# Optimization experiments

Hardware: AMD Instinct MI355X
Metric: run time of the kernel (lower is better)

## Reference

```python
import jax, jax.numpy as jnp
import numpy as np

L_LAYERS, D, H, FF_MUL = 4, 512, 8, 4
VOCAB, SEQ, MEM, CMEM, RATIO = 32000, 1024, 1024, 256, 4
DH = D // H


def _ln(x, g, b):
    mu = jnp.mean(x, -1, keepdims=True)
    var = jnp.mean((x - mu) ** 2, -1, keepdims=True)
    return (x - mu) / jnp.sqrt(var + 1e-5) * g + b


def _heads(x):
    b, n, _ = x.shape
    return x.reshape(b, n, H, -1).transpose(0, 2, 1, 3)  # [b,h,n,dh]


def _shift(x):
    # relative-position shift trick, x: [b,h,i,j] -> [b,h,i,j]
    b, h, i, j = x.shape
    x = jnp.concatenate([x, jnp.zeros((b, h, i, i), x.dtype)], -1)
    l = i + j - 1
    x = x.reshape(b, h, i * (i + j))
    pad = (-x.shape[-1]) % l
    x = jnp.pad(x, ((0, 0), (0, 0), (0, pad))).reshape(b, h, -1, l)
    return x[:, :, :i, i - 1:]


def _conv(x, w, b):
    # x: [B,L,D], w: [D_out, D_in, RATIO] (OIH), stride=RATIO
    y = jax.lax.conv_general_dilated(x.transpose(0, 2, 1), w, (RATIO,), 'VALID',
                                     dimension_numbers=('NCH', 'OIH', 'NCH'))
    return y.transpose(0, 2, 1) + b


def _full_attn(q, k, v):
    dots = jnp.einsum('bhid,bhjd->bhij', q, k) * (q.shape[-1] ** -0.5)
    return jnp.einsum('bhij,bhjd->bhid', jax.nn.softmax(dots, -1), v)


def setup_inputs() -> dict:
    key = jax.random.key(0)
    ks = jax.random.split(key, 24)
    s = 0.02
    return {
        'seq': jax.random.randint(ks[0], (4, SEQ), 0, VOCAB),
        'mask': jnp.ones((4, SEQ), dtype=bool),
        'mems': jax.random.normal(ks[1], (L_LAYERS, 4, MEM, D)) * s,
        'cmems': jax.random.normal(ks[2], (L_LAYERS, 4, CMEM, D)) * s,
        'pos_emb': jax.random.normal(ks[3], (H, CMEM + MEM + SEQ, DH)) * s,
        'embed': jax.random.normal(ks[4], (VOCAB, D)) * s,
        'ln1_g': jnp.ones((L_LAYERS, D)), 'ln1_b': jnp.zeros((L_LAYERS, D)),
        'Wq': jax.random.normal(ks[5], (L_LAYERS, D, D)) * s,
        'Wkv': jax.random.normal(ks[6], (L_LAYERS, D, 2 * D)) * s,
        'Wo': jax.random.normal(ks[7], (L_LAYERS, D, D)) * s,
        'bo': jnp.zeros((L_LAYERS, D)),
        'conv_w': jax.random.normal(ks[8], (L_LAYERS, D, D, RATIO)) * s,
        'conv_b': jnp.zeros((L_LAYERS, D)),
        'ln2_g': jnp.ones((L_LAYERS, D)), 'ln2_b': jnp.zeros((L_LAYERS, D)),
        'W1': jax.random.normal(ks[9], (L_LAYERS, D, FF_MUL * D)) * s,
        'b1': jnp.zeros((L_LAYERS, FF_MUL * D)),
        'W2': jax.random.normal(ks[10], (L_LAYERS, FF_MUL * D, D)) * s,
        'b2': jnp.zeros((L_LAYERS, D)),
    }


def _forward(seq, mask, mems, cmems, pos_emb, embed, ln1_g, ln1_b, Wq, Wkv, Wo, bo,
             conv_w, conv_b, ln2_g, ln2_b, W1, b1, W2, b2):
    scale = DH ** -0.5
    x = embed[seq]  # [b,t,d]
    maskb = mask.astype(bool)
    new_mems, new_cmems = [], []
    aux_total = jnp.zeros((), x.dtype)
    w_acc = 0.0
    for l in range(L_LAYERS):
        mem, cmem = mems[l], cmems[l]
        xn = _ln(x, ln1_g[l], ln1_b[l])
        q = _heads(xn @ Wq[l])
        kv_in = jnp.concatenate([cmem, mem, xn], 1)  # [b,kv_len,d]
        kv_len = kv_in.shape[1]
        k, v = jnp.split(kv_in @ Wkv[l], 2, -1)
        k, v = _heads(k), _heads(v)
        dots = jnp.einsum('bhid,bhjd->bhij', q, k) * scale
        pe = pos_emb[:, -kv_len:]
        dots = dots + _shift(jnp.einsum('bhid,hjd->bhij', q, pe) * scale)
        m2 = maskb[:, None, :, None] & maskb[:, None, None, :]  # [b,1,t,t]
        m2 = jnp.pad(m2, ((0, 0), (0, 0), (0, 0), (kv_len - SEQ, 0)), constant_values=True)
        dots = jnp.where(m2, dots, -jnp.finfo(dots.dtype).max)
        attn = jax.nn.softmax(dots, -1)
        w_acc = w_acc + jnp.mean(jax.lax.stop_gradient(attn), axis=(0, 1))
        out = jnp.einsum('bhij,bhjd->bhid', attn, v)
        out = out.transpose(0, 2, 1, 3).reshape(x.shape[0], SEQ, D)
        x = x + out @ Wo[l] + bo[l]
        # FIFO memory update (queue normed x, evict oldest)
        queue = jnp.concatenate([mem, xn], 1)
        old_mem, new_mem = queue[:, :-MEM], queue[:, -MEM:]
        pad_amt = old_mem.shape[1] % RATIO
        if pad_amt:
            old_mem = jnp.pad(old_mem, ((0, 0), (pad_amt, 0), (0, 0)))
        comp = _conv(old_mem, conv_w[l], conv_b[l])
        new_cmem = jnp.concatenate([cmem, comp], 1)[:, -CMEM:]
        new_mems.append(new_mem)
        new_cmems.append(new_cmem)
        # reconstruction (attention-reconstruction) aux loss
        old_mem_d = jax.lax.stop_gradient(old_mem)
        comp2 = _conv(old_mem_d, conv_w[l], conv_b[l])
        ck, cv = jnp.split(comp2 @ jax.lax.stop_gradient(Wkv[l]), 2, -1)
        ck, cv = _heads(ck), _heads(cv)
        start = kv_len - min(mem.shape[1], MEM) - SEQ
        ok = jax.lax.stop_gradient(k[:, :, start:kv_len - SEQ])
        ov = jax.lax.stop_gradient(v[:, :, start:kv_len - SEQ])
        qd = jax.lax.stop_gradient(q)
        aux_total = aux_total + jnp.mean((_full_attn(qd, ok, ov) - _full_attn(qd, ck, cv)) ** 2)
        # feed-forward block (PreNorm + Residual), exact GELU like torch nn.GELU
        xn2 = _ln(x, ln2_g[l], ln2_b[l])
        x = x + jax.nn.gelu(xn2 @ W1[l] + b1[l], approximate=False) @ W2[l] + b2[l]
    return (x, jnp.stack(new_mems), jnp.stack(new_cmems),
            aux_total / L_LAYERS, w_acc / L_LAYERS)


def reference(seq, mask, mems, cmems, pos_emb, embed, ln1_g, ln1_b, Wq, Wkv, Wo, bo,
              conv_w, conv_b, ln2_g, ln2_b, W1, b1, W2, b2):
    return _forward(seq, mask, mems, cmems, pos_emb, embed, ln1_g, ln1_b, Wq, Wkv, Wo, bo,
                    conv_w, conv_b, ln2_g, ln2_b, W1, b1, W2, b2)
```

## Files before the change

kernel.cpp:

```cpp
#include <hip/hip_runtime.h>
#include <hip/hip_bf16.h>


typedef __hip_bfloat16 bf16;
typedef short s16x8 __attribute__((ext_vector_type(8)));
typedef float f32x4 __attribute__((ext_vector_type(4)));

__device__ __forceinline__ f32x4 mfma16(s16x8 a, s16x8 b, f32x4 c) {
  return __builtin_amdgcn_mfma_f32_16x16x32_bf16(a, b, c, 0, 0, 0);
}

typedef __attribute__((address_space(1))) const void gvoid;
typedef __attribute__((address_space(3))) void lvoid;
__device__ __forceinline__ void gll16(const void* g, void* l) {
  __builtin_amdgcn_global_load_lds((gvoid*)g, (lvoid*)l, 16, 0, 0);
}

__device__ __forceinline__ float b2f(unsigned short u) {
  return __uint_as_float(((unsigned)u) << 16);
}
__device__ __forceinline__ unsigned short f2bb(float f) {
  bf16 h = __float2bfloat16(f);
  return *reinterpret_cast<unsigned short*>(&h);
}
__device__ __forceinline__ float ldf(const float* p) { return *p; }
__device__ __forceinline__ float ldf(const bf16* p) { return __bfloat162float(*p); }
__device__ __forceinline__ float4 ld4(const float* p) { return *(const float4*)p; }
__device__ __forceinline__ float4 ld4(const bf16* p) {
  const ushort4 u = *(const ushort4*)p;
  return make_float4(b2f(u.x), b2f(u.y), b2f(u.z), b2f(u.w));
}
__device__ __forceinline__ void st4(float* p, float4 r) { *(float4*)p = r; }
__device__ __forceinline__ void st4(bf16* p, float4 r) {
  *(ushort4*)p = make_ushort4(f2bb(r.x), f2bb(r.y), f2bb(r.z), f2bb(r.w));
}
__device__ __forceinline__ void stf(float* p, float v) { *p = v; }
__device__ __forceinline__ void stf(bf16* p, float v) { *p = __float2bfloat16(v); }

__global__ void probe_k(const void* ln1g, unsigned* flag) {
  if (threadIdx.x == 0) {
    const unsigned short u = *(const unsigned short*)ln1g;
    *flag = (u == 0x3F80u) ? 1u : 0u;
  }
}

template <int BM, int AMODE, bool ADD, bool BIAS, bool GELU, typename TC>
__global__ __launch_bounds__(256) void mgemm_k(
    const bf16* __restrict__ A, const int lda, const bf16* __restrict__ Bt,
    TC* __restrict__ C, const int ldc, const float* __restrict__ bias,
    const int K) {
  constexpr int NF = (BM == 128) ? 4 : 2;
  __shared__ bf16 As[BM * 64];
  __shared__ bf16 Bs[128 * 64];
  const int t = threadIdx.x, w = t >> 6, lane = t & 63;
  const int g = lane >> 4, li = lane & 15;
  const int m0 = blockIdx.y * BM, n0 = blockIdx.x << 7;
  const int wrow = (BM == 128) ? ((w >> 1) << 6) : 0;
  const int wcol = (BM == 128) ? ((w & 1) << 6) : (w << 5);
  f32x4 acc[4][NF];
#pragma unroll
  for (int mf = 0; mf < 4; mf++)
#pragma unroll
    for (int nf = 0; nf < NF; nf++)
#pragma unroll
      for (int e = 0; e < 4; e++) acc[mf][nf][e] = 0.f;
  constexpr int ACH = BM / 32;
  const int srow = lane >> 3, s8 = lane & 7;
  for (int k0 = 0; k0 < K; k0 += 64) {
    __syncthreads();
#pragma unroll
    for (int it = 0; it < ACH; it++) {
      const int chunk = w * ACH + it;
      const int row = (chunk << 3) + srow;
      const int k8 = s8 ^ (row & 7);
      const bf16* src;
      if constexpr (AMODE == 0) {
        src = A + (size_t)(m0 + row) * lda + k0 + (k8 << 3);
      } else if constexpr (AMODE == 1) {
        const int m = m0 + row;
        src = A + ((size_t)((m >> 8) * 2304 + 256) << 9) + (m & 255) * 2048 +
              k0 + (k8 << 3);
      } else {
        const int m = m0 + row;
        src = A + ((size_t)((m >> 10) * 2304 + 1280 + (m & 1023)) << 9) + k0 +
              (k8 << 3);
      }
      gll16(src, As + (chunk << 9));
    }
#pragma unroll
    for (int it = 0; it < 4; it++) {
      const int chunk = (w << 2) + it;
      const int row = (chunk << 3) + srow;
      const int k8 = s8 ^ (row & 7);
      gll16(Bt + (size_t)(n0 + row) * K + k0 + (k8 << 3), Bs + (chunk << 9));
    }
    __syncthreads();
#pragma unroll
    for (int ks = 0; ks < 2; ks++) {
      s16x8 af[4];
#pragma unroll
      for (int mf = 0; mf < 4; mf++) {
        const int row = wrow + (mf << 4) + li;
        af[mf] = *reinterpret_cast<const s16x8*>(
            As + (row << 6) + ((((ks << 2) + g) ^ (row & 7)) << 3));
      }
#pragma unroll
      for (int nf = 0; nf < NF; nf++) {
        const int col = wcol + (nf << 4) + li;
        const s16x8 bfr = *reinterpret_cast<const s16x8*>(
            Bs + (col << 6) + ((((ks << 2) + g) ^ (col & 7)) << 3));
#pragma unroll
        for (int mf = 0; mf < 4; mf++)
          acc[mf][nf] = mfma16(af[mf], bfr, acc[mf][nf]);
      }
    }
  }
#pragma unroll
  for (int mf = 0; mf < 4; mf++)
#pragma unroll
    for (int nf = 0; nf < NF; nf++) {
      const int n = n0 + wcol + (nf << 4) + li;
      const float bv = BIAS ? bias[n] : 0.f;
#pragma unroll
      for (int r = 0; r < 4; r++) {
        const int m = m0 + wrow + (mf << 4) + (g << 2) + r;
        float v = acc[mf][nf][r] + bv;
        if constexpr (GELU) v = 0.5f * v * (1.0f + erff(v * 0.70710678118f));
        TC* cp = C + (size_t)m * ldc + n;
        if constexpr (ADD)
          *cp += v;
        else
          stf(cp, v);
      }
    }
}

template <bool REL, bool DIFF, typename TO>
__global__ __launch_bounds__(256) void flash_k(
    const bf16* __restrict__ q, const bf16* __restrict__ kbase,
    const bf16* __restrict__ vbase, const int kvlen, const int ldkv,
    const int bstride, const bf16* __restrict__ pe,
    const bf16* __restrict__ zrow, float2* __restrict__ ml,
    TO* __restrict__ outp, const float* __restrict__ prior,
    float* __restrict__ auxsum) {
  __shared__ short k_s[2][4096];
  __shared__ short v_s[2][4096];
  __shared__ short p_s[4096];
  const int t = threadIdx.x, w = t >> 6, lane = t & 63;
  const int g = lane >> 4, li = lane & 15;
  const int bid = blockIdx.x;
  const int h = bid & 7;
  const int sl = bid >> 3;
  const int b = sl >> 4;
  const int i0 = (sl & 15) << 6;
  const bf16* qp =
      q + (size_t)(b * 1024 + i0 + (w << 4) + li) * 512 + (h << 6) + (g << 3);
  const s16x8 qf0 = *reinterpret_cast<const s16x8*>(qp);
  const s16x8 qf1 = *reinterpret_cast<const s16x8*>(qp + 32);
  const bf16* kpb = kbase + (size_t)b * bstride + (h << 6);
  const bf16* vpb = vbase + (size_t)b * bstride + (h << 6);
  const bf16* peh = REL ? pe + (size_t)h * 147456 : nullptr;
  const int vr = t >> 3, vc8 = t & 7;
  const int kr = lane >> 3, kc8 = lane & 7;
  float mreg[4] = {-1e30f, -1e30f, -1e30f, -1e30f};
  float lreg[4] = {0.f, 0.f, 0.f, 0.f};
  f32x4 o[4];
#pragma unroll
  for (int nt = 0; nt < 4; nt++)
#pragma unroll
    for (int e = 0; e < 4; e++) o[nt][e] = 0.f;

#define STAGE_K(J0, BUF)                                                      \
  {                                                                           \
    _Pragma("unroll") for (int it = 0; it < 2; it++) {                        \
      const int chunk = (w << 1) + it;                                        \
      const int row = (chunk << 3) + kr;                                      \
      gll16(kpb + (size_t)((J0) + row) * ldkv + ((kc8 ^ (row & 7)) << 3),     \
            &k_s[BUF][chunk << 9]);                                           \
    }                                                                         \
  }
#define LOAD_V(J0, VA, VB)                                                    \
  {                                                                           \
    VA = *reinterpret_cast<const s16x8*>(                                     \
        vpb + (size_t)((J0) + vr) * ldkv + (vc8 << 3));                       \
    VB = *reinterpret_cast<const s16x8*>(                                     \
        vpb + (size_t)((J0) + 32 + vr) * ldkv + (vc8 << 3));                  \
  }
#define WRITE_V(BUF, VA, VB)                                                  \
  {                                                                           \
    _Pragma("unroll") for (int e = 0; e < 8; e++) {                           \
      const int d = (vc8 << 3) + e;                                           \
      const int sw = ((vc8 ^ e) & 7) << 3;                                    \
      v_s[BUF][((d << 6) + vr) ^ sw] = VA[e];                                 \
      v_s[BUF][((d << 6) + (vr + 32)) ^ sw] = VB[e];                          \
    }                                                                         \
  }

  {
    s16x8 va, vb2;
    STAGE_K(0, 0);
    LOAD_V(0, va, vb2);
    WRITE_V(0, va, vb2);
    __syncthreads();
  }
  int cur = 0;
  for (int j0 = 0; j0 < kvlen; j0 += 64) {
    const bool last = (j0 + 64 >= kvlen);
    s16x8 nva, nvb;
    if (!last) {
      LOAD_V(j0 + 64, nva, nvb);
      STAGE_K(j0 + 64, cur ^ 1);
    }
    const int ub0 = j0 - i0 + 960;
    const bool doT = REL && (ub0 < 2304);
    s16x8 pb[5][2];
    if (REL && doT) {
      const int ubase = j0 - i0 + 1008 - (w << 4);
#pragma unroll
      for (int ut = 0; ut < 5; ut++) {
        const int u = ubase + (ut << 4) + li;
        const bf16* pp = (u < 2304) ? peh + ((size_t)u << 6) : zrow;
        pb[ut][0] = *reinterpret_cast<const s16x8*>(pp + (g << 3));
        pb[ut][1] = *reinterpret_cast<const s16x8*>(pp + 32 + (g << 3));
      }
    }
    f32x4 s[4];
#pragma unroll
    for (int nt = 0; nt < 4; nt++) {
#pragma unroll
      for (int e = 0; e < 4; e++) s[nt][e] = 0.f;
      const int j = (nt << 4) + li;
      const s16x8 kb0 = *reinterpret_cast<const s16x8*>(
          &k_s[cur][(j << 6) + ((g ^ (j & 7)) << 3)]);
      const s16x8 kb1 = *reinterpret_cast<const s16x8*>(
          &k_s[cur][(j << 6) + (((g + 4) ^ (j & 7)) << 3)]);
      s[nt] = mfma16(qf0, kb0, s[nt]);
      s[nt] = mfma16(qf1, kb1, s[nt]);
    }
    if (REL && doT) {
      f32x4 t5[5];
#pragma unroll
      for (int ut = 0; ut < 5; ut++) {
#pragma unroll
        for (int e = 0; e < 4; e++) t5[ut][e] = 0.f;
        t5[ut] = mfma16(qf0, pb[ut][0], t5[ut]);
        t5[ut] = mfma16(qf1, pb[ut][1], t5[ut]);
      }
#pragma unroll
      for (int r = 0; r < 4; r++) {
        const int il = (g << 2) + r;
        const int local = li - il + 15;
        const int srcl = (g << 4) | (local & 15);
        float tv[5];
#pragma unroll
        for (int ut = 0; ut < 5; ut++) tv[ut] = __shfl(t5[ut][r], srcl);
        const bool hi = local >= 16;
#pragma unroll
        for (int nt = 0; nt < 4; nt++) s[nt][r] += hi ? tv[nt + 1] : tv[nt];
      }
    }
#pragma unroll
    for (int nt = 0; nt < 4; nt++)
#pragma unroll
      for (int e = 0; e < 4; e++) s[nt][e] *= 0.125f;
    float pr[4][4];
#pragma unroll
    for (int r = 0; r < 4; r++) {
      float tm = fmaxf(fmaxf(s[0][r], s[1][r]), fmaxf(s[2][r], s[3][r]));
#pragma unroll
      for (int off = 1; off < 16; off <<= 1) tm = fmaxf(tm, __shfl_xor(tm, off));
      const float mn = fmaxf(mreg[r], tm);
      const float al = __expf(mreg[r] - mn);
      mreg[r] = mn;
      float te = 0.f;
#pragma unroll
      for (int nt = 0; nt < 4; nt++) {
        pr[nt][r] = __expf(s[nt][r] - mn);
        te += pr[nt][r];
      }
#pragma unroll
      for (int off = 1; off < 16; off <<= 1) te += __shfl_xor(te, off);
      lreg[r] = lreg[r] * al + te;
#pragma unroll
      for (int nt = 0; nt < 4; nt++) o[nt][r] *= al;
    }
    short* pw = p_s + (w << 10);
#pragma unroll
    for (int nt = 0; nt < 4; nt++)
#pragma unroll
      for (int r = 0; r < 4; r++) {
        const int il = (g << 2) + r;
        pw[((il << 6) + (nt << 4) + li) ^ ((il & 7) << 3)] = (short)f2bb(pr[nt][r]);
      }
#pragma unroll
    for (int ks = 0; ks < 2; ks++) {
      const s16x8 pa = *reinterpret_cast<const s16x8*>(
          pw + (((li << 6) + (ks << 5) + (g << 3)) ^ ((li & 7) << 3)));
#pragma unroll
      for (int nt = 0; nt < 4; nt++) {
        const int d = (nt << 4) + li;
        const s16x8 vb = *reinterpret_cast<const s16x8*>(
            &v_s[cur][((d << 6) + (ks << 5) + (g << 3)) ^
                      ((((d >> 3) ^ (d & 7)) & 7) << 3)]);
        o[nt] = mfma16(pa, vb, o[nt]);
      }
    }
    if (!last) WRITE_V(cur ^ 1, nva, nvb);
    __syncthreads();
    cur ^= 1;
  }
#undef STAGE_K
#undef LOAD_V
#undef WRITE_V
  float rl[4];
#pragma unroll
  for (int r = 0; r < 4; r++) rl[r] = 1.0f / lreg[r];
  if constexpr (REL) {
    if (li == 0) {
#pragma unroll
      for (int r = 0; r < 4; r++)
        ml[(size_t)((b << 3) + h) * 1024 + i0 + (w << 4) + (g << 2) + r] =
            make_float2(mreg[r], lreg[r]);
    }
  }
  if constexpr (!DIFF) {
#pragma unroll
    for (int nt = 0; nt < 4; nt++)
#pragma unroll
      for (int r = 0; r < 4; r++) {
        const size_t adr = (size_t)(b * 1024 + i0 + (w << 4) + (g << 2) + r) * 512 +
                           (h << 6) + (nt << 4) + li;
        stf(outp + adr, o[nt][r] * rl[r]);
      }
  } else {
    float sq = 0.f;
#pragma unroll
    for (int nt = 0; nt < 4; nt++)
#pragma unroll
      for (int r = 0; r < 4; r++) {
        const size_t adr = (size_t)(b * 1024 + i0 + (w << 4) + (g << 2) + r) * 512 +
                           (h << 6) + (nt << 4) + li;
        const float dv = o[nt][r] * rl[r] - prior[adr];
        sq = fmaf(dv, dv, sq);
      }
#pragma unroll
    for (int off = 1; off < 64; off <<= 1) sq += __shfl_xor(sq, off);
    float* fl = reinterpret_cast<float*>(p_s);
    if (lane == 0) fl[w] = sq;
    __syncthreads();
    if (t == 0) atomicAdd(auxsum, fl[0] + fl[1] + fl[2] + fl[3]);
  }
}

__global__ __launch_bounds__(256) void wacc_k(const bf16* __restrict__ q,
                                              const bf16* __restrict__ kv,
                                              const bf16* __restrict__ pe,
                                              const bf16* __restrict__ zrow,
                                              const float2* __restrict__ ml,
                                              float* __restrict__ w_acc) {
  __shared__ short k_s[2][4096];
  const int t = threadIdx.x, w = t >> 6, lane = t & 63;
  const int g = lane >> 4, li = lane & 15;
  const int i0 = blockIdx.x << 6, j0 = blockIdx.y << 6;
  const int ub0 = j0 - i0 + 960;
  const bool doT = (ub0 < 2304);
  const int kr = lane >> 3, kc8 = lane & 7;
  f32x4 acc[4];
#pragma unroll
  for (int nt = 0; nt < 4; nt++)
#pragma unroll
    for (int e = 0; e < 4; e++) acc[nt][e] = 0.f;

#define STAGE_KW(HB, BUF)                                                     \
  {                                                                           \
    const int hh = (HB) >> 2, bb = (HB)&3;                                    \
    const bf16* kpb = kv + (size_t)bb * 2359296 + (hh << 6);                  \
    _Pragma("unroll") for (int it = 0; it < 2; it++) {                        \
      const int chunk = (w << 1) + it;                                        \
      const int row = (chunk << 3) + kr;                                      \
      gll16(kpb + (size_t)(j0 + row) * 1024 + ((kc8 ^ (row & 7)) << 3),       \
            &k_s[BUF][chunk << 9]);                                           \
    }                                                                         \
  }
  STAGE_KW(0, 0);
  __syncthreads();
  int cur = 0;
  for (int hb = 0; hb < 32; hb++) {
    const int h = hb >> 2, b = hb & 3;
    if (hb < 31) STAGE_KW(hb + 1, cur ^ 1);
    const bf16* qp =
        q + (size_t)(b * 1024 + i0 + (w << 4) + li) * 512 + (h << 6) + (g << 3);
    const s16x8 qf0 = *reinterpret_cast<const s16x8*>(qp);
    const s16x8 qf1 = *reinterpret_cast<const s16x8*>(qp + 32);
    s16x8 pb[5][2];
    if (doT) {
      const bf16* peh = pe + (size_t)h * 147456;
      const int ubase = j0 - i0 + 1008 - (w << 4);
#pragma unroll
      for (int ut = 0; ut < 5; ut++) {
        const int u = ubase + (ut << 4) + li;
        const bf16* pp = (u < 2304) ? peh + ((size_t)u << 6) : zrow;
        pb[ut][0] = *reinterpret_cast<const s16x8*>(pp + (g << 3));
        pb[ut][1] = *reinterpret_cast<const s16x8*>(pp + 32 + (g << 3));
      }
    }
    f32x4 s[4];
#pragma unroll
    for (int nt = 0; nt < 4; nt++) {
#pragma unroll
      for (int e = 0; e < 4; e++) s[nt][e] = 0.f;
      const int j = (nt << 4) + li;
      const s16x8 kb0 = *reinterpret_cast<const s16x8*>(
          &k_s[cur][(j << 6) + ((g ^ (j & 7)) << 3)]);
      const s16x8 kb1 = *reinterpret_cast<const s16x8*>(
          &k_s[cur][(j << 6) + (((g + 4) ^ (j & 7)) << 3)]);
      s[nt] = mfma16(qf0, kb0, s[nt]);
      s[nt] = mfma16(qf1, kb1, s[nt]);
    }
    if (doT) {
      f32x4 t5[5];
#pragma unroll
      for (int ut = 0; ut < 5; ut++) {
#pragma unroll
        for (int e = 0; e < 4; e++) t5[ut][e] = 0.f;
        t5[ut] = mfma16(qf0, pb[ut][0], t5[ut]);
        t5[ut] = mfma16(qf1, pb[ut][1], t5[ut]);
      }
#pragma unroll
      for (int r = 0; r < 4; r++) {
        const int il = (g << 2) + r;
        const int local = li - il + 15;
        const int srcl = (g << 4) | (local & 15);
        float tv[5];
#pragma unroll
        for (int ut = 0; ut < 5; ut++) tv[ut] = __shfl(t5[ut][r], srcl);
        const bool hi = local >= 16;
#pragma unroll
        for (int nt = 0; nt < 4; nt++) s[nt][r] += hi ? tv[nt + 1] : tv[nt];
      }
    }
#pragma unroll
    for (int r = 0; r < 4; r++) {
      const float2 st =
          ml[(size_t)((b << 3) + h) * 1024 + i0 + (w << 4) + (g << 2) + r];
      const float rr = 1.0f / st.y;
#pragma unroll
      for (int nt = 0; nt < 4; nt++)
        acc[nt][r] += __expf(s[nt][r] * 0.125f - st.x) * rr;
    }
    __syncthreads();
    cur ^= 1;
  }
#undef STAGE_KW
#pragma unroll
  for (int nt = 0; nt < 4; nt++)
#pragma unroll
    for (int r = 0; r < 4; r++) {
      float* wp = w_acc + (size_t)(i0 + (w << 4) + (g << 2) + r) * 2304 + j0 +
                  (nt << 4) + li;
      *wp += acc[nt][r];
    }
}

template <typename TIN>
__global__ __launch_bounds__(256) void wtr_k(
    const TIN* __restrict__ Wq, const TIN* __restrict__ Wkv,
    const TIN* __restrict__ Wo, const TIN* __restrict__ W1,
    const TIN* __restrict__ W2, bf16* __restrict__ WT,
    const unsigned* flag, unsigned want) {
  if (*flag != want) return;
  __shared__ bf16 tile[64][65];
  int bx = blockIdx.x;
  const TIN* W;
  bf16* dst;
  int N, K;
  if (bx < 64) {
    W = Wq; dst = WT; N = 512; K = 512;
  } else if (bx < 192) {
    W = Wkv; dst = WT + 262144; N = 1024; K = 512; bx -= 64;
  } else if (bx < 256) {
    W = Wo; dst = WT + 786432; N = 512; K = 512; bx -= 192;
  } else if (bx < 512) {
    W = W1; dst = WT + 1048576; N = 2048; K = 512; bx -= 256;
  } else {
    W = W2; dst = WT + 2097152; N = 512; K = 2048; bx -= 512;
  }
  const int tn = N >> 6;
  const int kt = bx / tn, nt = bx - kt * tn;
  const int k0 = kt << 6, n0 = nt << 6;
  const int t = threadIdx.x;
#pragma unroll
  for (int i = 0; i < 16; i++) {
    const int idx = (i << 8) + t;
    const int kr = idx >> 6, nc = idx & 63;
    tile[kr][nc] = __float2bfloat16(ldf(W + (size_t)(k0 + kr) * N + n0 + nc));
  }
  __syncthreads();
#pragma unroll
  for (int i = 0; i < 16; i++) {
    const int idx = (i << 8) + t;
    const int nr = idx >> 6, kc = idx & 63;
    dst[(size_t)(n0 + nr) * K + k0 + kc] = tile[kc][nr];
  }
}

template <typename TIN>
__global__ void wcp_k(const TIN* __restrict__ cw, bf16* __restrict__ WcT,
                      const unsigned* flag, unsigned want) {
  if (*flag != want) return;
  const int id = blockIdx.x * 256 + threadIdx.x;
  const int o = id >> 11, p = id & 2047;
  const int r = p >> 9, i = p & 511;
  WcT[id] = __float2bfloat16(ldf(cw + ((size_t)o << 11) + (i << 2) + r));
}

template <typename TIN>
__global__ void kvb_k(const TIN* __restrict__ cmem, const TIN* __restrict__ mem,
                      bf16* __restrict__ kvin, const unsigned* flag, unsigned want) {
  if (*flag != want) return;
  const int id = blockIdx.x * 256 + threadIdx.x;
  const int row = id >> 7, c4 = (id & 127) << 2;
  const int b = row / 1280, j = row - b * 1280;
  const TIN* src = (j < 256) ? cmem + (((size_t)(b * 256 + j)) << 9) + c4
                             : mem + (((size_t)(b * 1024 + j - 256)) << 9) + c4;
  st4(kvin + (((size_t)(b * 2304 + j)) << 9) + c4, ld4(src));
}

template <typename TIN>
__global__ void bcvt_k(const TIN* __restrict__ bo, const TIN* __restrict__ cb,
                       const TIN* __restrict__ b1, const TIN* __restrict__ b2,
                       float* __restrict__ bws, const unsigned* flag, unsigned want) {
  if (*flag != want) return;
  const int id = blockIdx.x * 256 + threadIdx.x;
  const int l = id / 3584, r = id - l * 3584;
  float v;
  if (r < 512) v = ldf(bo + l * 512 + r);
  else if (r < 1024) v = ldf(cb + l * 512 + r - 512);
  else if (r < 3072) v = ldf(b1 + l * 2048 + r - 1024);
  else v = ldf(b2 + l * 512 + r - 3072);
  bws[id] = v;
}

template <typename TIN, typename TY>
__global__ __launch_bounds__(256) void ln_k(const float* __restrict__ x,
                                            const TIN* __restrict__ g,
                                            const TIN* __restrict__ bta,
                                            TY* __restrict__ y, bf16* kvx,
                                            const unsigned* flag, unsigned want) {
  if (*flag != want) return;
  const int w = threadIdx.x >> 6, lane = threadIdx.x & 63;
  const size_t row = (size_t)blockIdx.x * 4 + w;
  const float* xr = x + row * 512;
  float v[8], s = 0, ss = 0;
#pragma unroll
  for (int i = 0; i < 8; i++) {
    v[i] = xr[lane + (i << 6)];
    s += v[i];
    ss = fmaf(v[i], v[i], ss);
  }
#pragma unroll
  for (int off = 1; off < 64; off <<= 1) {
    s += __shfl_xor(s, off);
    ss += __shfl_xor(ss, off);
  }
  const float mu = s * (1.0f / 512.0f);
  const float var = ss * (1.0f / 512.0f) - mu * mu;
  const float inv = rsqrtf(var + 1e-5f);
  bf16* k2 = kvx ? kvx + (((row >> 10) * 2304 + 1280 + (row & 1023)) << 9) : nullptr;
#pragma unroll
  for (int i = 0; i < 8; i++) {
    const int c = lane + (i << 6);
    const float val = (v[i] - mu) * inv * ldf(g + c) + ldf(bta + c);
    stf(y + row * 512 + c, val);
    if (k2) k2[c] = __float2bfloat16(val);
  }
}

template <typename TIN>
__global__ void embed_k(const int* __restrict__ seq, const TIN* __restrict__ emb,
                        float* __restrict__ x, const unsigned* flag, unsigned want) {
  if (*flag != want) return;
  const int row = blockIdx.x;
  const int tok = seq[row];
  const TIN* e = emb + (size_t)tok * 512;
  float* xr = x + (size_t)row * 512;
  for (int c = threadIdx.x; c < 512; c += 256) xr[c] = ldf(e + c);
}

template <typename TIN>
__global__ void cvtpe_k(const TIN* __restrict__ pe, bf16* __restrict__ peb,
                        const unsigned* flag, unsigned want) {
  if (*flag != want) return;
  const int i = blockIdx.x * 256 + threadIdx.x;
  peb[i] = __float2bfloat16(ldf(pe + i));
}

__global__ void zero_k(float* __restrict__ p, int n) {
  for (int i = blockIdx.x * 256 + threadIdx.x; i < n; i += gridDim.x * 256) p[i] = 0.0f;
}

template <typename TOUT>
__global__ void cpy_k(const bf16* __restrict__ s, TOUT* __restrict__ d, int n,
                      const unsigned* flag, unsigned want) {
  if (*flag != want) return;
  for (int i = blockIdx.x * 256 + threadIdx.x; i < n; i += gridDim.x * 256)
    stf(d + i, ldf(s + i));
}

template <typename TOUT>
__global__ void f2bs_k(const float* __restrict__ s, TOUT* __restrict__ d, float sc,
                       int n, const unsigned* flag, unsigned want) {
  if (*flag != want) return;
  for (int i = blockIdx.x * 256 + threadIdx.x; i < n; i += gridDim.x * 256)
    stf(d + i, s[i] * sc);
}

template <typename TOUT>
__global__ void fin_aux_k(const float* __restrict__ acc, TOUT* __restrict__ d,
                          const unsigned* flag, unsigned want) {
  if (*flag != want) return;
  if (threadIdx.x == 0) stf(d, acc[0] * (1.0f / 8388608.0f));
}

extern "C" void kernel_launch(void* const* d_in, const int* in_sizes, int n_in,
                              void* d_out, int out_size, void* d_ws, size_t ws_size,
                              hipStream_t stream) {
  typedef const bf16 CB;
  typedef const float CF;
  const int* seq = (const int*)d_in[0];
  CB *mems_b = (CB*)d_in[2], *cmems_b = (CB*)d_in[3], *pe_b = (CB*)d_in[4],
     *emb_b = (CB*)d_in[5], *l1g_b = (CB*)d_in[6], *l1b_b = (CB*)d_in[7],
     *Wq_b = (CB*)d_in[8], *Wkv_b = (CB*)d_in[9], *Wo_b = (CB*)d_in[10],
     *bo_b = (CB*)d_in[11], *cw_b = (CB*)d_in[12], *cb_b = (CB*)d_in[13],
     *l2g_b = (CB*)d_in[14], *l2b_b = (CB*)d_in[15], *W1_b = (CB*)d_in[16],
     *b1_b = (CB*)d_in[17], *W2_b = (CB*)d_in[18], *b2_b = (CB*)d_in[19];
  CF *mems_f = (CF*)d_in[2], *cmems_f = (CF*)d_in[3], *pe_f = (CF*)d_in[4],
     *emb_f = (CF*)d_in[5], *l1g_f = (CF*)d_in[6], *l1b_f = (CF*)d_in[7],
     *Wq_f = (CF*)d_in[8], *Wkv_f = (CF*)d_in[9], *Wo_f = (CF*)d_in[10],
     *bo_f = (CF*)d_in[11], *cw_f = (CF*)d_in[12], *cb_f = (CF*)d_in[13],
     *l2g_f = (CF*)d_in[14], *l2b_f = (CF*)d_in[15], *W1_f = (CF*)d_in[16],
     *b1_f = (CF*)d_in[17], *W2_f = (CF*)d_in[18], *b2_f = (CF*)d_in[19];
  bf16* outb = (bf16*)d_out;
  float* outf = (float*)d_out;

  float* ws = (float*)d_ws;
  float* x = ws;
  bf16* q = (bf16*)(ws + 2097152);
  bf16* kv = (bf16*)(ws + 3145728);
  bf16* mid = (bf16*)(ws + 3145728);
  float* region = ws + 7864320;
  bf16* attn_o = (bf16*)region;
  bf16* xn2 = (bf16*)region;
  bf16* ckcv = (bf16*)(ws + 9961472);
  float* w_acc = ws + 10485760;
  bf16* cmp_ws = (bf16*)(ws + 12845056);
  float2* ml = (float2*)(ws + 13369344);
  float* auxsum = ws + 13434880;
  unsigned* flag = (unsigned*)(ws + 13434881);
  bf16* pe_w = (bf16*)(ws + 13434884);
  float* bias_ws = ws + 14024708;
  bf16* kvin = (bf16*)(ws + 14039044);
  bf16* WT = (bf16*)(ws + 16398340);
  float* aux1 = ws + 18757636;
  float* zrow_f = ws + 20854788;
  bf16* zrow = (bf16*)zrow_f;

  probe_k<<<1, 64, 0, stream>>>(d_in[6], flag);
  zero_k<<<2048, 256, 0, stream>>>(w_acc, 2359296);
  zero_k<<<1, 256, 0, stream>>>(auxsum, 1);
  zero_k<<<1, 64, 0, stream>>>(zrow_f, 32);
  embed_k<bf16><<<4096, 256, 0, stream>>>(seq, emb_b, x, flag, 1);
  embed_k<float><<<4096, 256, 0, stream>>>(seq, emb_f, x, flag, 0);
  cvtpe_k<bf16><<<4608, 256, 0, stream>>>(pe_b, pe_w, flag, 1);
  cvtpe_k<float><<<4608, 256, 0, stream>>>(pe_f, pe_w, flag, 0);
  bcvt_k<bf16><<<56, 256, 0, stream>>>(bo_b, cb_b, b1_b, b2_b, bias_ws, flag, 1);
  bcvt_k<float><<<56, 256, 0, stream>>>(bo_f, cb_f, b1_f, b2_f, bias_ws, flag, 0);

  for (int l = 0; l < 4; l++) {
    bf16* xnl_b = outb + 2097152 + (size_t)l * 2097152;
    float* xnl_f = outf + 2097152 + (size_t)l * 2097152;
    bf16* cmp_b = outb + 10485760 + (size_t)l * 524288;
    float* cmp_f = outf + 10485760 + (size_t)l * 524288;
    const float* bl = bias_ws + l * 3584;

    wtr_k<bf16><<<768, 256, 0, stream>>>(Wq_b + (size_t)l * 262144,
        Wkv_b + (size_t)l * 524288, Wo_b + (size_t)l * 262144,
        W1_b + (size_t)l * 1048576, W2_b + (size_t)l * 1048576, WT, flag, 1);
    wtr_k<float><<<768, 256, 0, stream>>>(Wq_f + (size_t)l * 262144,
        Wkv_f + (size_t)l * 524288, Wo_f + (size_t)l * 262144,
        W1_f + (size_t)l * 1048576, W2_f + (size_t)l * 1048576, WT, flag, 0);
    wcp_k<bf16><<<4096, 256, 0, stream>>>(cw_b + (size_t)l * 1048576, WT + 3145728, flag, 1);
    wcp_k<float><<<4096, 256, 0, stream>>>(cw_f + (size_t)l * 1048576, WT + 3145728, flag, 0);
    kvb_k<bf16><<<2560, 256, 0, stream>>>(cmems_b + (size_t)l * 524288,
                                          mems_b + (size_t)l * 2097152, kvin, flag, 1);
    kvb_k<float><<<2560, 256, 0, stream>>>(cmems_f + (size_t)l * 524288,
                                           mems_f + (size_t)l * 2097152, kvin, flag, 0);
    ln_k<bf16, bf16><<<1024, 256, 0, stream>>>(x, l1g_b + l * 512, l1b_b + l * 512,
                                               xnl_b, kvin, flag, 1);
    ln_k<float, float><<<1024, 256, 0, stream>>>(x, l1g_f + l * 512, l1b_f + l * 512,
                                                 xnl_f, kvin, flag, 0);
    mgemm_k<64, 2, false, false, false, bf16><<<dim3(4, 64), 256, 0, stream>>>(
        kvin, 512, WT, q, 512, nullptr, 512);
    mgemm_k<128, 0, false, false, false, bf16><<<dim3(8, 72), 256, 0, stream>>>(
        kvin, 512, WT + 262144, kv, 1024, nullptr, 512);
    flash_k<true, false, bf16><<<512, 256, 0, stream>>>(
        q, kv, kv + 512, 2304, 1024, 2359296, pe_w, zrow, ml, attn_o,
        nullptr, nullptr);
    wacc_k<<<dim3(16, 36), 256, 0, stream>>>(q, kv, pe_w, zrow, ml, w_acc);
    mgemm_k<64, 0, true, true, false, float><<<dim3(4, 64), 256, 0, stream>>>(
        attn_o, 512, WT + 786432, x, 512, bl, 512);
    mgemm_k<64, 1, false, true, false, bf16><<<dim3(4, 16), 256, 0, stream>>>(
        kvin, 0, WT + 3145728, cmp_ws, 512, bl + 512, 2048);
    cpy_k<bf16><<<512, 256, 0, stream>>>(cmp_ws, cmp_b, 524288, flag, 1);
    cpy_k<float><<<512, 256, 0, stream>>>(cmp_ws, cmp_f, 524288, flag, 0);
    mgemm_k<64, 0, false, false, false, bf16><<<dim3(8, 16), 256, 0, stream>>>(
        cmp_ws, 512, WT + 262144, ckcv, 1024, nullptr, 512);
    flash_k<false, false, float><<<512, 256, 0, stream>>>(
        q, kv + 262144, kv + 262144 + 512, 1024, 1024, 2359296, nullptr, zrow,
        nullptr, aux1, nullptr, nullptr);
    flash_k<false, true, float><<<512, 256, 0, stream>>>(
        q, ckcv, ckcv + 512, 256, 1024, 262144, nullptr, zrow, nullptr,
        (float*)nullptr, aux1, auxsum);
    ln_k<bf16, bf16><<<1024, 256, 0, stream>>>(x, l2g_b + l * 512, l2b_b + l * 512,
                                               xn2, nullptr, flag, 1);
    ln_k<float, bf16><<<1024, 256, 0, stream>>>(x, l2g_f + l * 512, l2b_f + l * 512,
                                                xn2, nullptr, flag, 0);
    mgemm_k<128, 0, false, true, true, bf16><<<dim3(16, 32), 256, 0, stream>>>(
        xn2, 512, WT + 1048576, mid, 2048, bl + 1024, 512);
    mgemm_k<64, 0, true, true, false, float><<<dim3(4, 64), 256, 0, stream>>>(
        mid, 2048, WT + 2097152, x, 512, bl + 3072, 2048);
  }

  f2bs_k<bf16><<<2048, 256, 0, stream>>>(x, outb, 1.0f, 2097152, flag, 1);
  f2bs_k<float><<<2048, 256, 0, stream>>>(x, outf, 1.0f, 2097152, flag, 0);
  f2bs_k<bf16><<<2048, 256, 0, stream>>>(w_acc, outb + 12582913, 1.0f / 128.0f, 2359296, flag, 1);
  f2bs_k<float><<<2048, 256, 0, stream>>>(w_acc, outf + 12582913, 1.0f / 128.0f, 2359296, flag, 0);
  fin_aux_k<bf16><<<1, 64, 0, stream>>>(auxsum, outb + 12582912, flag, 1);
  fin_aux_k<float><<<1, 64, 0, stream>>>(auxsum, outf + 12582912, flag, 0);
}
```

Baseline: 2.342 ms.

## Fuse aux-loss attention passes into one kernel and restructure wacc scheduling

Two aux-loss flash passes (old memory and compressed memory) are merged into one kernel. It keeps both outputs in registers and computes the squared difference directly, so the fp32 intermediate buffer no longer needs a write and a read-back. wacc_k gets a 1D grid remapped so each XCD handles particular key tiles, loads the positional-embedding fragments only once per head, and prefetches the next head/batch q and softmax stats. The fused kernel is single-buffered with no K/V prefetch overlap, which may cost some latency hiding.

```diff
diff --git a/kernel.cpp b/kernel.cpp
--- a/kernel.cpp
+++ b/kernel.cpp
@@ -135,14 +135,12 @@
     }
 }
 
-template <bool REL, bool DIFF, typename TO>
 __global__ __launch_bounds__(256) void flash_k(
     const bf16* __restrict__ q, const bf16* __restrict__ kbase,
     const bf16* __restrict__ vbase, const int kvlen, const int ldkv,
     const int bstride, const bf16* __restrict__ pe,
     const bf16* __restrict__ zrow, float2* __restrict__ ml,
-    TO* __restrict__ outp, const float* __restrict__ prior,
-    float* __restrict__ auxsum) {
+    bf16* __restrict__ outp) {
   __shared__ short k_s[2][4096];
   __shared__ short v_s[2][4096];
   __shared__ short p_s[4096];
@@ -159,7 +157,7 @@
   const s16x8 qf1 = *reinterpret_cast<const s16x8*>(qp + 32);
   const bf16* kpb = kbase + (size_t)b * bstride + (h << 6);
   const bf16* vpb = vbase + (size_t)b * bstride + (h << 6);
-  const bf16* peh = REL ? pe + (size_t)h * 147456 : nullptr;
+  const bf16* peh = pe + (size_t)h * 147456;
   const int vr = t >> 3, vc8 = t & 7;
   const int kr = lane >> 3, kc8 = lane & 7;
   float mreg[4] = {-1e30f, -1e30f, -1e30f, -1e30f};
@@ -212,9 +210,9 @@
       STAGE_K(j0 + 64, cur ^ 1);
     }
     const int ub0 = j0 - i0 + 960;
-    const bool doT = REL && (ub0 < 2304);
+    const bool doT = (ub0 < 2304);
     s16x8 pb[5][2];
-    if (REL && doT) {
+    if (doT) {
       const int ubase = j0 - i0 + 1008 - (w << 4);
 #pragma unroll
       for (int ut = 0; ut < 5; ut++) {
@@ -237,7 +235,7 @@
       s[nt] = mfma16(qf0, kb0, s[nt]);
       s[nt] = mfma16(qf1, kb1, s[nt]);
     }
-    if (REL && doT) {
+    if (doT) {
       f32x4 t5[5];
 #pragma unroll
       for (int ut = 0; ut < 5; ut++) {
@@ -315,41 +313,168 @@
   float rl[4];
 #pragma unroll
   for (int r = 0; r < 4; r++) rl[r] = 1.0f / lreg[r];
-  if constexpr (REL) {
-    if (li == 0) {
-#pragma unroll
-      for (int r = 0; r < 4; r++)
-        ml[(size_t)((b << 3) + h) * 1024 + i0 + (w << 4) + (g << 2) + r] =
-            make_float2(mreg[r], lreg[r]);
-    }
-  }
-  if constexpr (!DIFF) {
-#pragma unroll
-    for (int nt = 0; nt < 4; nt++)
+  if (li == 0) {
+#pragma unroll
+    for (int r = 0; r < 4; r++)
+      ml[(size_t)((b << 3) + h) * 1024 + i0 + (w << 4) + (g << 2) + r] =
+          make_float2(mreg[r], lreg[r]);
+  }
+#pragma unroll
+  for (int nt = 0; nt < 4; nt++)
+#pragma unroll
+    for (int r = 0; r < 4; r++) {
+      const size_t adr = (size_t)(b * 1024 + i0 + (w << 4) + (g << 2) + r) * 512 +
+                         (h << 6) + (nt << 4) + li;
+      stf(outp + adr, o[nt][r] * rl[r]);
+    }
+}
+
+__global__ __launch_bounds__(256) void auxf_k(
+    const bf16* __restrict__ q, const bf16* __restrict__ k1,
+    const bf16* __restrict__ v1, const bf16* __restrict__ k2,
+    const bf16* __restrict__ v2, float* __restrict__ auxsum) {
+  __shared__ short k_s[4096];
+  __shared__ short v_s[4096];
+  __shared__ short p_s[4096];
+  const int t = threadIdx.x, w = t >> 6, lane = t & 63;
+  const int g = lane >> 4, li = lane & 15;
+  const int bid = blockIdx.x;
+  const int h = bid & 7;
+  const int sl = bid >> 3;
+  const int b = sl >> 4;
+  const int i0 = (sl & 15) << 6;
+  const bf16* qp =
+      q + (size_t)(b * 1024 + i0 + (w << 4) + li) * 512 + (h << 6) + (g << 3);
+  const s16x8 qf0 = *reinterpret_cast<const s16x8*>(qp);
+  const s16x8 qf1 = *reinterpret_cast<const s16x8*>(qp + 32);
+  const bf16* kbs[2] = {k1 + (size_t)b * 2359296 + (h << 6),
+                        k2 + (size_t)b * 262144 + (h << 6)};
+  const bf16* vbs[2] = {v1 + (size_t)b * 2359296 + (h << 6),
+                        v2 + (size_t)b * 262144 + (h << 6)};
+  const int vr = t >> 3, vc8 = t & 7;
+  const int kr = lane >> 3, kc8 = lane & 7;
+  float ms[2][4], ls[2][4];
+  f32x4 o[2][4];
+#pragma unroll
+  for (int sg = 0; sg < 2; sg++)
+#pragma unroll
+    for (int r = 0; r < 4; r++) {
+      ms[sg][r] = -1e30f;
+      ls[sg][r] = 0.f;
+#pragma unroll
+      for (int e = 0; e < 4; e++) o[sg][r][e] = 0.f;
+    }
+#pragma unroll
+  for (int sg = 0; sg < 2; sg++) {
+    const bf16* kbp = kbs[sg];
+    const bf16* vbp = vbs[sg];
+    const int NT = sg ? 4 : 16;
+    for (int jt = 0; jt < NT; jt++) {
+      const int j0 = jt << 6;
+      __syncthreads();
+      {
+#pragma unroll
+        for (int it = 0; it < 2; it++) {
+          const int chunk = (w << 1) + it;
+          const int row = (chunk << 3) + kr;
+          gll16(kbp + (size_t)(j0 + row) * 1024 + ((kc8 ^ (row & 7)) << 3),
+                &k_s[chunk << 9]);
+        }
+        const s16x8 va = *reinterpret_cast<const s16x8*>(
+            vbp + (size_t)(j0 + vr) * 1024 + (vc8 << 3));
+        const s16x8 vb2 = *reinterpret_cast<const s16x8*>(
+            vbp + (size_t)(j0 + 32 + vr) * 1024 + (vc8 << 3));
+#pragma unroll
+        for (int e = 0; e < 8; e++) {
+          const int d = (vc8 << 3) + e;
+          const int sw = ((vc8 ^ e) & 7) << 3;
+          v_s[((d << 6) + vr) ^ sw] = va[e];
+          v_s[((d << 6) + (vr + 32)) ^ sw] = vb2[e];
+        }
+      }
+      __syncthreads();
+      f32x4 s[4];
+#pragma unroll
+      for (int nt = 0; nt < 4; nt++) {
+#pragma unroll
+        for (int e = 0; e < 4; e++) s[nt][e] = 0.f;
+        const int j = (nt << 4) + li;
+        const s16x8 kb0 = *reinterpret_cast<const s16x8*>(
+            &k_s[(j << 6) + ((g ^ (j & 7)) << 3)]);
+        const s16x8 kb1 = *reinterpret_cast<const s16x8*>(
+            &k_s[(j << 6) + (((g + 4) ^ (j & 7)) << 3)]);
+        s[nt] = mfma16(qf0, kb0, s[nt]);
+        s[nt] = mfma16(qf1, kb1, s[nt]);
+      }
+      float pr[4][4];
 #pragma unroll
       for (int r = 0; r < 4; r++) {
-        const size_t adr = (size_t)(b * 1024 + i0 + (w << 4) + (g << 2) + r) * 512 +
-                           (h << 6) + (nt << 4) + li;
-        stf(outp + adr, o[nt][r] * rl[r]);
-      }
-  } else {
-    float sq = 0.f;
-#pragma unroll
-    for (int nt = 0; nt < 4; nt++)
-#pragma unroll
-      for (int r = 0; r < 4; r++) {
-        const size_t adr = (size_t)(b * 1024 + i0 + (w << 4) + (g << 2) + r) * 512 +
-                           (h << 6) + (nt << 4) + li;
-        const float dv = o[nt][r] * rl[r] - prior[adr];
-        sq = fmaf(dv, dv, sq);
-      }
-#pragma unroll
-    for (int off = 1; off < 64; off <<= 1) sq += __shfl_xor(sq, off);
-    float* fl = reinterpret_cast<float*>(p_s);
-    if (lane == 0) fl[w] = sq;
-    __syncthreads();
-    if (t == 0) atomicAdd(auxsum, fl[0] + fl[1] + fl[2] + fl[3]);
-  }
+        float sv[4];
+#pragma unroll
+        for (int nt = 0; nt < 4; nt++) sv[nt] = s[nt][r] * 0.125f;
+        float tm = fmaxf(fmaxf(sv[0], sv[1]), fmaxf(sv[2], sv[3]));
+#pragma unroll
+        for (int off = 1; off < 16; off <<= 1) tm = fmaxf(tm, __shfl_xor(tm, off));
+        const float mn = fmaxf(ms[sg][r], tm);
+        const float al = __expf(ms[sg][r] - mn);
+        ms[sg][r] = mn;
+        float te = 0.f;
+#pragma unroll
+        for (int nt = 0; nt < 4; nt++) {
+          pr[nt][r] = __expf(sv[nt] - mn);
+          te += pr[nt][r];
+        }
+#pragma unroll
+        for (int off = 1; off < 16; off <<= 1) te += __shfl_xor(te, off);
+        ls[sg][r] = ls[sg][r] * al + te;
+#pragma unroll
+        for (int nt = 0; nt < 4; nt++) o[sg][nt][r] *= al;
+      }
+      short* pw = p_s + (w << 10);
+#pragma unroll
+      for (int nt = 0; nt < 4; nt++)
+#pragma unroll
+        for (int r = 0; r < 4; r++) {
+          const int il = (g << 2) + r;
+          pw[((il << 6) + (nt << 4) + li) ^ ((il & 7) << 3)] =
+              (short)f2bb(pr[nt][r]);
+        }
+#pragma unroll
+      for (int ks = 0; ks < 2; ks++) {
+        const s16x8 pa = *reinterpret_cast<const s16x8*>(
+            pw + (((li << 6) + (ks << 5) + (g << 3)) ^ ((li & 7) << 3)));
+#pragma unroll
+        for (int nt = 0; nt < 4; nt++) {
+          const int d = (nt << 4) + li;
+          const s16x8 vb = *reinterpret_cast<const s16x8*>(
+              &v_s[((d << 6) + (ks << 5) + (g << 3)) ^
+                   ((((d >> 3) ^ (d & 7)) & 7) << 3)]);
+          o[sg][nt] = mfma16(pa, vb, o[sg][nt]);
+        }
+      }
+    }
+  }
+  float rl0[4], rl1[4];
+#pragma unroll
+  for (int r = 0; r < 4; r++) {
+    rl0[r] = 1.0f / ls[0][r];
+    rl1[r] = 1.0f / ls[1][r];
+  }
+  float sq = 0.f;
+#pragma unroll
+  for (int nt = 0; nt < 4; nt++)
+#pragma unroll
+    for (int r = 0; r < 4; r++) {
+      const float dv = o[0][nt][r] * rl0[r] - o[1][nt][r] * rl1[r];
+      sq = fmaf(dv, dv, sq);
+    }
+#pragma unroll
+  for (int off = 1; off < 64; off <<= 1) sq += __shfl_xor(sq, off);
+  float* fl = reinterpret_cast<float*>(p_s);
+  __syncthreads();
+  if (lane == 0) fl[w] = sq;
+  __syncthreads();
+  if (t == 0) atomicAdd(auxsum, fl[0] + fl[1] + fl[2] + fl[3]);
 }
 
 __global__ __launch_bounds__(256) void wacc_k(const bf16* __restrict__ q,
@@ -361,7 +486,11 @@
   __shared__ short k_s[2][4096];
   const int t = threadIdx.x, w = t >> 6, lane = t & 63;
   const int g = lane >> 4, li = lane & 15;
-  const int i0 = blockIdx.x << 6, j0 = blockIdx.y << 6;
+  const int bid = blockIdx.x;
+  const int xcd = bid & 7, idx = bid >> 3;
+  const int j0t = ((idx >> 4) << 3) + xcd;
+  if (j0t >= 36) return;
+  const int i0 = (idx & 15) << 6, j0 = j0t << 6;
   const int ub0 = j0 - i0 + 960;
   const bool doT = (ub0 < 2304);
   const int kr = lane >> 3, kc8 = lane & 7;
@@ -382,18 +511,33 @@
             &k_s[BUF][chunk << 9]);                                           \
     }                                                                         \
   }
+#define LOADQ(HB, Q0, Q1)                                                     \
+  {                                                                           \
+    const int hh = (HB) >> 2, bb = (HB)&3;                                    \
+    const bf16* qpp = q + (size_t)(bb * 1024 + i0 + (w << 4) + li) * 512 +    \
+                      (hh << 6) + (g << 3);                                   \
+    Q0 = *reinterpret_cast<const s16x8*>(qpp);                                \
+    Q1 = *reinterpret_cast<const s16x8*>(qpp + 32);                           \
+  }
+#define LOADML(HB, DST)                                                       \
+  {                                                                           \
+    const int hh = (HB) >> 2, bb = (HB)&3;                                    \
+    _Pragma("unroll") for (int r = 0; r < 4; r++) DST[r] =                    \
+        ml[(size_t)((bb << 3) + hh) * 1024 + i0 + (w << 4) + (g << 2) + r];   \
+  }
+
   STAGE_KW(0, 0);
+  s16x8 qf0, qf1;
+  float2 mlr[4];
+  LOADQ(0, qf0, qf1);
+  LOADML(0, mlr);
+  s16x8 pb[5][2];
   __syncthreads();
   int cur = 0;
   for (int hb = 0; hb < 32; hb++) {
-    const int h = hb >> 2, b = hb & 3;
+    const int h = hb >> 2;
     if (hb < 31) STAGE_KW(hb + 1, cur ^ 1);
-    const bf16* qp =
-        q + (size_t)(b * 1024 + i0 + (w << 4) + li) * 512 + (h << 6) + (g << 3);
-    const s16x8 qf0 = *reinterpret_cast<const s16x8*>(qp);
-    const s16x8 qf1 = *reinterpret_cast<const s16x8*>(qp + 32);
-    s16x8 pb[5][2];
-    if (doT) {
+    if (doT && (hb & 3) == 0) {
       const bf16* peh = pe + (size_t)h * 147456;
       const int ubase = j0 - i0 + 1008 - (w << 4);
 #pragma unroll
@@ -403,6 +547,12 @@
         pb[ut][0] = *reinterpret_cast<const s16x8*>(pp + (g << 3));
         pb[ut][1] = *reinterpret_cast<const s16x8*>(pp + 32 + (g << 3));
       }
+    }
+    s16x8 qn0, qn1;
+    float2 mln[4];
+    if (hb < 31) {
+      LOADQ(hb + 1, qn0, qn1);
+      LOADML(hb + 1, mln);
     }
     f32x4 s[4];
 #pragma unroll
@@ -441,17 +591,23 @@
     }
 #pragma unroll
     for (int r = 0; r < 4; r++) {
-      const float2 st =
-          ml[(size_t)((b << 3) + h) * 1024 + i0 + (w << 4) + (g << 2) + r];
-      const float rr = 1.0f / st.y;
+      const float rr = 1.0f / mlr[r].y;
 #pragma unroll
       for (int nt = 0; nt < 4; nt++)
-        acc[nt][r] += __expf(s[nt][r] * 0.125f - st.x) * rr;
+        acc[nt][r] += __expf(s[nt][r] * 0.125f - mlr[r].x) * rr;
     }
     __syncthreads();
     cur ^= 1;
+    if (hb < 31) {
+      qf0 = qn0;
+      qf1 = qn1;
+#pragma unroll
+      for (int r = 0; r < 4; r++) mlr[r] = mln[r];
+    }
   }
 #undef STAGE_KW
+#undef LOADQ
+#undef LOADML
 #pragma unroll
   for (int nt = 0; nt < 4; nt++)
 #pragma unroll
@@ -661,8 +817,7 @@
   float* bias_ws = ws + 14024708;
   bf16* kvin = (bf16*)(ws + 14039044);
   bf16* WT = (bf16*)(ws + 16398340);
-  float* aux1 = ws + 18757636;
-  float* zrow_f = ws + 20854788;
+  float* zrow_f = ws + 18757636;
   bf16* zrow = (bf16*)zrow_f;
 
   probe_k<<<1, 64, 0, stream>>>(d_in[6], flag);
@@ -703,10 +858,9 @@
         kvin, 512, WT, q, 512, nullptr, 512);
     mgemm_k<128, 0, false, false, false, bf16><<<dim3(8, 72), 256, 0, stream>>>(
         kvin, 512, WT + 262144, kv, 1024, nullptr, 512);
-    flash_k<true, false, bf16><<<512, 256, 0, stream>>>(
-        q, kv, kv + 512, 2304, 1024, 2359296, pe_w, zrow, ml, attn_o,
-        nullptr, nullptr);
-    wacc_k<<<dim3(16, 36), 256, 0, stream>>>(q, kv, pe_w, zrow, ml, w_acc);
+    flash_k<<<512, 256, 0, stream>>>(q, kv, kv + 512, 2304, 1024, 2359296,
+                                     pe_w, zrow, ml, attn_o);
+    wacc_k<<<640, 256, 0, stream>>>(q, kv, pe_w, zrow, ml, w_acc);
     mgemm_k<64, 0, true, true, false, float><<<dim3(4, 64), 256, 0, stream>>>(
         attn_o, 512, WT + 786432, x, 512, bl, 512);
     mgemm_k<64, 1, false, true, false, bf16><<<dim3(4, 16), 256, 0, stream>>>(
@@ -715,12 +869,8 @@
     cpy_k<float><<<512, 256, 0, stream>>>(cmp_ws, cmp_f, 524288, flag, 0);
     mgemm_k<64, 0, false, false, false, bf16><<<dim3(8, 16), 256, 0, stream>>>(
         cmp_ws, 512, WT + 262144, ckcv, 1024, nullptr, 512);
-    flash_k<false, false, float><<<512, 256, 0, stream>>>(
-        q, kv + 262144, kv + 262144 + 512, 1024, 1024, 2359296, nullptr, zrow,
-        nullptr, aux1, nullptr, nullptr);
-    flash_k<false, true, float><<<512, 256, 0, stream>>>(
-        q, ckcv, ckcv + 512, 256, 1024, 262144, nullptr, zrow, nullptr,
-        (float*)nullptr, aux1, auxsum);
+    auxf_k<<<512, 256, 0, stream>>>(q, kv + 262144, kv + 262144 + 512,
+                                    ckcv, ckcv + 512, auxsum);
     ln_k<bf16, bf16><<<1024, 256, 0, stream>>>(x, l2g_b + l * 512, l2b_b + l * 512,
                                                xn2, nullptr, flag, 1);
     ln_k<float, bf16><<<1024, 256, 0, stream>>>(x, l2g_f + l * 512, l2b_f + l * 512,
```

Result: faster. 2.049 ms (-12.5%).
